# Optimization experiments

Measured on AMD Instinct MI355X. Metric: run time of the kernel, lower is better.

The kernel has to match this reference:

```python
import jax, jax.numpy as jnp
import numpy as np

CODEBOOK_SIZE = 1024
CODEBOOK_DIM = 64
COMMITMENT_WEIGHT = 0.25
DECAY = 0.99
EPS = 1e-5


def setup_inputs() -> dict:
    key = jax.random.key(0)
    k1, k2, k3 = jax.random.split(key, 3)
    B, D, T = 32, CODEBOOK_DIM, 4096
    z = jax.random.normal(k1, (B, D, T), dtype=jnp.float32)
    embedding = jax.random.normal(k2, (CODEBOOK_SIZE, CODEBOOK_DIM), dtype=jnp.float32)
    cluster_size = jnp.zeros((CODEBOOK_SIZE,), dtype=jnp.float32)
    embed_avg = jax.random.normal(k3, (CODEBOOK_SIZE, CODEBOOK_DIM), dtype=jnp.float32)
    return {"z": z, "embedding": embedding, "cluster_size": cluster_size, "embed_avg": embed_avg}


def reference(z, embedding, cluster_size, embed_avg):
    # z: [B, D, T]; embedding/embed_avg: [K, D]; cluster_size: [K]
    B, D, T = z.shape
    K = embedding.shape[0]
    z_flat = jnp.transpose(z, (0, 2, 1)).reshape(-1, D)  # [N, D], N = B*T

    # squared-euclidean distances via expansion (matches torch cdist expansion)
    dist = (
        jnp.sum(z_flat * z_flat, axis=1, keepdims=True)
        + jnp.sum(embedding * embedding, axis=1)
        - 2.0 * (z_flat @ embedding.T)
    )  # [N, K]
    indices = jnp.argmin(dist, axis=1)  # [N] int

    # EMA updates (training path). one_hot.sum(0) -> segment count; one_hot.T @ z_flat -> segment sum
    counts = jax.ops.segment_sum(jnp.ones(z_flat.shape[0], dtype=z_flat.dtype), indices, num_segments=K)
    new_cluster_size = cluster_size * DECAY + (1.0 - DECAY) * counts
    embed_sum = jax.ops.segment_sum(z_flat, indices, num_segments=K)  # [K, D]
    new_embed_avg = embed_avg * DECAY + (1.0 - DECAY) * embed_sum
    n = jnp.sum(new_cluster_size)
    smoothed = (new_cluster_size + EPS) / (n + K * EPS) * n  # Laplace smoothing
    new_embedding = new_embed_avg / smoothed[:, None]  # [K, D]

    # quantize with the *updated* codebook (as in the torch in-place update)
    z_q_flat = new_embedding[indices]  # [N, D] gather
    loss = COMMITMENT_WEIGHT * jnp.mean((z_flat - jax.lax.stop_gradient(z_q_flat)) ** 2)
    # straight-through estimator
    z_q_flat = z_flat + jax.lax.stop_gradient(z_q_flat - z_flat)
    z_q = jnp.transpose(z_q_flat.reshape(B, T, D), (0, 2, 1))  # [B, D, T]
    return z_q, loss, indices.reshape(B, T)
```

## Files before the change

kernel.cpp:

```cpp
#include <hip/hip_runtime.h>

#define N_PTS 131072
#define TD 4096
#define DD 64
#define KK 1024
#define MARGIN_TH 2e-3f

typedef short bf16x8 __attribute__((ext_vector_type(8)));
typedef float f32x4  __attribute__((ext_vector_type(4)));

__device__ inline unsigned short f2bf(float f) {
    unsigned u = __float_as_uint(f);
    unsigned r = u + 0x7FFFu + ((u >> 16) & 1u);
    return (unsigned short)(r >> 16);
}
__device__ inline float bf2f(unsigned short h) {
    return __uint_as_float(((unsigned)h) << 16);
}

__device__ inline void gload_lds16(const unsigned short* g, unsigned short* l) {
    __builtin_amdgcn_global_load_lds(
        (const __attribute__((address_space(1))) unsigned int*)g,
        (__attribute__((address_space(3))) unsigned int*)l, 16, 0, 0);
}

__global__ __launch_bounds__(256) void vq_prep(const float* __restrict__ z,
                                               unsigned short* __restrict__ zh,
                                               unsigned short* __restrict__ zl)
{
    __shared__ float tile[64][65];
    const int tid = threadIdx.x;
    const int b = blockIdx.x >> 6;
    const int t0 = (blockIdx.x & 63) * 64;

    const int d = tid >> 2, tq = tid & 3;
#pragma unroll
    for (int it = 0; it < 4; ++it) {
        const int tt = tq * 16 + it * 4;
        const float4 v = *(const float4*)(z + ((size_t)b * DD + d) * TD + t0 + tt);
        tile[d][tt] = v.x; tile[d][tt + 1] = v.y; tile[d][tt + 2] = v.z; tile[d][tt + 3] = v.w;
    }
    __syncthreads();

    const int p = tid >> 2, dg = tid & 3;
    bf16x8 h0, h1, l0, l1;
#pragma unroll
    for (int j = 0; j < 8; ++j) {
        const float v0 = -tile[dg * 16 + j][p];
        const unsigned short a = f2bf(v0);
        h0[j] = (short)a; l0[j] = (short)f2bf(v0 - bf2f(a));
        const float v1 = -tile[dg * 16 + 8 + j][p];
        const unsigned short c = f2bf(v1);
        h1[j] = (short)c; l1[j] = (short)f2bf(v1 - bf2f(c));
    }
    const size_t o = ((size_t)(b * TD + t0 + p)) * DD + dg * 16;
    *(bf16x8*)(zh + o) = h0;
    *(bf16x8*)(zh + o + 8) = h1;
    *(bf16x8*)(zl + o) = l0;
    *(bf16x8*)(zl + o + 8) = l1;
}

__global__ __launch_bounds__(256) void vq_eprep(const float* __restrict__ emb,
                                                unsigned short* __restrict__ eh,
                                                unsigned short* __restrict__ el,
                                                float* __restrict__ halfnorm)
{
    const int k = blockIdx.x * 256 + threadIdx.x;
    if (k >= KK) return;
    const float* e = emb + (size_t)k * DD;
    double s = 0.0;
#pragma unroll
    for (int d = 0; d < DD; ++d) {
        const float v = e[d];
        const double dv = (double)v;
        s = fma(dv, dv, s);
        const unsigned short h = f2bf(v);
        eh[(size_t)k * DD + d] = h;
        el[(size_t)k * DD + d] = f2bf(v - bf2f(h));
    }
    halfnorm[k] = (float)(0.5 * s);
}

__global__ __launch_bounds__(256, 4) void vq_screen_mfma(
    const unsigned short* __restrict__ zh, const unsigned short* __restrict__ zl,
    const unsigned short* __restrict__ eh, const unsigned short* __restrict__ el,
    const float* __restrict__ hn,
    int* __restrict__ idx_ws, float* __restrict__ ind_out,
    int* __restrict__ nflag, int* __restrict__ flags, int* __restrict__ hist)
{
    __shared__ __align__(16) unsigned short ehs[2][1024];
    __shared__ __align__(16) unsigned short els[2][1024];

    const int tid  = threadIdx.x;
    const int lane = tid & 63;
    const int wv   = tid >> 6;
    const int quad = lane >> 4;
    const int col  = lane & 15;
    const int pbase = blockIdx.x * 128 + wv * 32;

    const bf16x8* pA0h = (const bf16x8*)(zh + (size_t)(pbase + col) * DD + quad * 8);
    const bf16x8* pA0l = (const bf16x8*)(zl + (size_t)(pbase + col) * DD + quad * 8);
    const bf16x8* pA1h = (const bf16x8*)(zh + (size_t)(pbase + 16 + col) * DD + quad * 8);
    const bf16x8* pA1l = (const bf16x8*)(zl + (size_t)(pbase + 16 + col) * DD + quad * 8);
    const bf16x8 A0h0 = pA0h[0], A0h1 = pA0h[4];
    const bf16x8 A0l0 = pA0l[0], A0l1 = pA0l[4];
    const bf16x8 A1h0 = pA1h[0], A1h1 = pA1h[4];
    const bf16x8 A1l0 = pA1l[0], A1l1 = pA1l[4];

    const int ci = tid & 127;
    const int sc = ci >> 3, sm = ci & 7;
    const int sj = (sm - sc) & 7;
    const unsigned short* sgl = (tid < 128 ? eh : el) + sc * DD + sj * 8;
    unsigned short* dst0 = (tid < 128 ? &ehs[0][0] : &els[0][0]) + (wv & 1) * 512 + lane * 8;
    unsigned short* dst1 = dst0 + 1024;

    const int pH0 = (col * 8 + ((quad + col) & 7)) * 8;
    const int pH1 = (col * 8 + ((quad + 4 + col) & 7)) * 8;

    gload_lds16(sgl, dst0);
    float hnv_c = hn[col];
    float hnv_n = hnv_c;
    __syncthreads();

    float best0[4]  = {1e30f, 1e30f, 1e30f, 1e30f};
    float best20[4] = {1e30f, 1e30f, 1e30f, 1e30f};
    int   bidx0[4]  = {0, 0, 0, 0};
    float best1[4]  = {1e30f, 1e30f, 1e30f, 1e30f};
    float best21[4] = {1e30f, 1e30f, 1e30f, 1e30f};
    int   bidx1[4]  = {0, 0, 0, 0};

    int code = col;
#pragma unroll 2
    for (int t = 0; t < KK / 16; ++t) {
        const int cur = t & 1;
        if (t < 63) {
            gload_lds16(sgl + (t + 1) * (16 * DD), cur ? dst0 : dst1);
            hnv_n = hn[(t + 1) * 16 + col];
        }

        const unsigned short* bh = &ehs[cur][0];
        const unsigned short* bl = &els[cur][0];
        const bf16x8 Bh0 = *(const bf16x8*)(bh + pH0);
        const bf16x8 Bh1 = *(const bf16x8*)(bh + pH1);
        const bf16x8 Bl0 = *(const bf16x8*)(bl + pH0);
        const bf16x8 Bl1 = *(const bf16x8*)(bl + pH1);

        f32x4 a0 = {hnv_c, hnv_c, hnv_c, hnv_c};
        f32x4 a1 = {hnv_c, hnv_c, hnv_c, hnv_c};
        a0 = __builtin_amdgcn_mfma_f32_16x16x32_bf16(A0h0, Bh0, a0, 0, 0, 0);
        a1 = __builtin_amdgcn_mfma_f32_16x16x32_bf16(A1h0, Bh0, a1, 0, 0, 0);
        a0 = __builtin_amdgcn_mfma_f32_16x16x32_bf16(A0h1, Bh1, a0, 0, 0, 0);
        a1 = __builtin_amdgcn_mfma_f32_16x16x32_bf16(A1h1, Bh1, a1, 0, 0, 0);
        a0 = __builtin_amdgcn_mfma_f32_16x16x32_bf16(A0l0, Bh0, a0, 0, 0, 0);
        a1 = __builtin_amdgcn_mfma_f32_16x16x32_bf16(A1l0, Bh0, a1, 0, 0, 0);
        a0 = __builtin_amdgcn_mfma_f32_16x16x32_bf16(A0l1, Bh1, a0, 0, 0, 0);
        a1 = __builtin_amdgcn_mfma_f32_16x16x32_bf16(A1l1, Bh1, a1, 0, 0, 0);
        a0 = __builtin_amdgcn_mfma_f32_16x16x32_bf16(A0h0, Bl0, a0, 0, 0, 0);
        a1 = __builtin_amdgcn_mfma_f32_16x16x32_bf16(A1h0, Bl0, a1, 0, 0, 0);
        a0 = __builtin_amdgcn_mfma_f32_16x16x32_bf16(A0h1, Bl1, a0, 0, 0, 0);
        a1 = __builtin_amdgcn_mfma_f32_16x16x32_bf16(A1h1, Bl1, a1, 0, 0, 0);

#pragma unroll
        for (int r = 0; r < 4; ++r) {
            const float s0 = a0[r];
            best20[r] = __builtin_amdgcn_fmed3f(best0[r], best20[r], s0);
            if (s0 < best0[r]) { best0[r] = s0; bidx0[r] = code; }
            const float s1 = a1[r];
            best21[r] = __builtin_amdgcn_fmed3f(best1[r], best21[r], s1);
            if (s1 < best1[r]) { best1[r] = s1; bidx1[r] = code; }
        }

        __syncthreads();
        hnv_c = hnv_n;
        code += 16;
    }

#pragma unroll
    for (int off = 1; off < 16; off <<= 1) {
#pragma unroll
        for (int r = 0; r < 4; ++r) {
            {
                const float ob  = __shfl_xor(best0[r],  off, 64);
                const float ob2 = __shfl_xor(best20[r], off, 64);
                const int   oi  = __shfl_xor(bidx0[r],  off, 64);
                const float nb2 = fminf(fminf(best20[r], ob2), fmaxf(best0[r], ob));
                if (ob < best0[r]) { best0[r] = ob; bidx0[r] = oi; }
                best20[r] = nb2;
            }
            {
                const float ob  = __shfl_xor(best1[r],  off, 64);
                const float ob2 = __shfl_xor(best21[r], off, 64);
                const int   oi  = __shfl_xor(bidx1[r],  off, 64);
                const float nb2 = fminf(fminf(best21[r], ob2), fmaxf(best1[r], ob));
                if (ob < best1[r]) { best1[r] = ob; bidx1[r] = oi; }
                best21[r] = nb2;
            }
        }
    }

    if (col == 0) {
#pragma unroll
        for (int r = 0; r < 4; ++r) {
            const int n0 = pbase + quad * 4 + r;
            idx_ws[n0] = bidx0[r];
            ind_out[n0] = (float)bidx0[r];
            atomicAdd(&hist[bidx0[r]], 1);
            if (best20[r] - best0[r] < MARGIN_TH) {
                const int pos = atomicAdd(nflag, 1);
                flags[pos] = n0;
            }
            const int n1 = pbase + 16 + quad * 4 + r;
            idx_ws[n1] = bidx1[r];
            ind_out[n1] = (float)bidx1[r];
            atomicAdd(&hist[bidx1[r]], 1);
            if (best21[r] - best1[r] < MARGIN_TH) {
                const int pos = atomicAdd(nflag, 1);
                flags[pos] = n1;
            }
        }
    }
}

__global__ __launch_bounds__(256) void vq_fallback(
    const float* __restrict__ z, const float* __restrict__ emb,
    int* __restrict__ idx_ws, float* __restrict__ ind_out,
    const int* __restrict__ nflag, const int* __restrict__ flags,
    int* __restrict__ hist)
{
    __shared__ float zs[4][DD];
    const int total = *nflag;
    const int lane = threadIdx.x & 63;
    const int wid = threadIdx.x >> 6;
    const int gw = blockIdx.x * 4 + wid;

    for (int i = gw; i < total; i += gridDim.x * 4) {
        const int n = flags[i];
        const int b = n >> 12, t = n & 4095;
        zs[wid][lane] = z[((size_t)b * DD + lane) * TD + t];
        __builtin_amdgcn_s_waitcnt(0);
        double best = 1e300;
        int bi = KK;
        for (int kc = 0; kc < KK / 64; ++kc) {
            const int k = kc * 64 + lane;
            const float4* e = (const float4*)(emb + (size_t)k * DD);
            double dot = 0.0, nn = 0.0;
#pragma unroll
            for (int j = 0; j < 16; ++j) {
                float4 ev = e[j];
                double e0 = (double)ev.x, e1 = (double)ev.y, e2 = (double)ev.z, e3 = (double)ev.w;
                nn = fma(e0, e0, fma(e1, e1, fma(e2, e2, fma(e3, e3, nn))));
                dot = fma((double)zs[wid][4 * j + 0], e0,
                      fma((double)zs[wid][4 * j + 1], e1,
                      fma((double)zs[wid][4 * j + 2], e2,
                      fma((double)zs[wid][4 * j + 3], e3, dot))));
            }
            double s = 0.5 * nn - dot;
            if (s < best || (s == best && k < bi)) { best = s; bi = k; }
        }
        for (int off = 32; off > 0; off >>= 1) {
            double os = __shfl_down(best, off, 64);
            int oi = __shfl_down(bi, off, 64);
            if (os < best || (os == best && oi < bi)) { best = os; bi = oi; }
        }
        if (lane == 0) {
            const int old = idx_ws[n];
            if (bi != old) {
                idx_ws[n] = bi;
                ind_out[n] = (float)bi;
                atomicAdd(&hist[old], -1);
                atomicAdd(&hist[bi], 1);
            }
        }
    }
}

__global__ __launch_bounds__(1024) void vq_prefix_smo(
    const int* __restrict__ hist, const float* __restrict__ cs,
    int* __restrict__ cursor, float* __restrict__ rsmo)
{
    __shared__ int tmp[KK];
    __shared__ double dred[KK];
    const int k = threadIdx.x;
    const int c = hist[k];
    tmp[k] = c;
    const double ncs = 0.99 * (double)cs[k] + 0.01 * (double)c;
    dred[k] = ncs;
    __syncthreads();
    for (int off = 1; off < KK; off <<= 1) {
        int u = (k >= off) ? tmp[k - off] : 0;
        __syncthreads();
        tmp[k] += u;
        __syncthreads();
    }
    cursor[k] = tmp[k] - c;
    for (int s = 512; s > 0; s >>= 1) {
        if (k < s) dred[k] += dred[k + s];
        __syncthreads();
    }
    const double nsum = dred[0];
    const double smo = (ncs + 1e-5) / (nsum + (double)KK * 1e-5) * nsum;
    rsmo[k] = (float)(1.0 / smo);
}

__global__ __launch_bounds__(256) void vq_scatter(const int* __restrict__ idx_ws,
                                                  int* __restrict__ cursor, int* __restrict__ order)
{
    const int n = blockIdx.x * 256 + threadIdx.x;
    const int bi = idx_ws[n];
    const int pos = atomicAdd(&cursor[bi], 1);
    order[pos] = n;
}

__global__ __launch_bounds__(256) void vq_esum2(
    const unsigned short* __restrict__ zh, const unsigned short* __restrict__ zl,
    const int* __restrict__ idx_ws, const int* __restrict__ order,
    float* __restrict__ esum)
{
    const int tid = threadIdx.x;
    const int lane = tid & 63;
    const int w = tid >> 6;
    const int base = blockIdx.x * 256 + w * 64;

    const int pid_l = order[base + lane];
    const int code_l = idx_ws[pid_l];

    float v[64];
#pragma unroll
    for (int j = 0; j < 64; ++j) {
        const int pj = __shfl(pid_l, j, 64);
        const size_t o = (size_t)pj * DD + lane;
        v[j] = bf2f(zh[o]) + bf2f(zl[o]);
    }

    float racc = 0.f;
    int cur = __shfl(code_l, 0, 64);
#pragma unroll
    for (int j = 0; j < 64; ++j) {
        const int cj = __shfl(code_l, j, 64);
        if (cj != cur) {
            atomicAdd(&esum[(size_t)cur * DD + lane], -racc);
            racc = 0.f;
            cur = cj;
        }
        racc += v[j];
    }
    atomicAdd(&esum[(size_t)cur * DD + lane], -racc);
}

__global__ __launch_bounds__(256) void vq_newE(
    const float* __restrict__ avg, const float* __restrict__ esum,
    const float* __restrict__ rsmo, float* __restrict__ newE)
{
    const int j = blockIdx.x * 256 + threadIdx.x;
    newE[j] = (float)((0.99 * (double)avg[j] + 0.01 * (double)esum[j]) * (double)rsmo[j >> 6]);
}

__global__ __launch_bounds__(256) void vq_gather_loss(
    const float* __restrict__ z, const float* __restrict__ newE,
    const int* __restrict__ idx_ws, float* __restrict__ zq_out,
    double* __restrict__ loss_acc, int* __restrict__ done_cnt,
    float* __restrict__ loss_out)
{
    const int tid = threadIdx.x;
    const int n = blockIdx.x * 256 + tid;
    const int b = n >> 12;
    const int t = n & 4095;
    const float* zb = z + ((size_t)b * DD) * TD + t;
    float* ob = zq_out + ((size_t)b * DD) * TD + t;
    const int bi = idx_ws[n];
    const float* e = newE + (size_t)bi * DD;
    double acc = 0.0;
#pragma unroll
    for (int d = 0; d < DD; ++d) {
        float q = e[d];
        float zv = zb[(size_t)d * TD];
        ob[(size_t)d * TD] = q;
        float df = zv - q;
        acc = fma((double)df, (double)df, acc);
    }
    for (int off = 32; off > 0; off >>= 1) acc += __shfl_down(acc, off, 64);
    __shared__ double wsum[4];
    const int wid = tid >> 6, lane = tid & 63;
    if (lane == 0) wsum[wid] = acc;
    __syncthreads();
    if (tid == 0) {
        atomicAdd(loss_acc, wsum[0] + wsum[1] + wsum[2] + wsum[3]);
        __threadfence();
        const int prev = atomicAdd(done_cnt, 1);
        if (prev == gridDim.x - 1) {
            __threadfence();
            *loss_out = (float)(0.25 * (*loss_acc) / (double)(N_PTS * DD));
        }
    }
}

extern "C" void kernel_launch(void* const* d_in, const int* in_sizes, int n_in,
                              void* d_out, int out_size, void* d_ws, size_t ws_size,
                              hipStream_t stream) {
    const float* z    = (const float*)d_in[0];
    const float* emb  = (const float*)d_in[1];
    const float* cs   = (const float*)d_in[2];
    const float* avg  = (const float*)d_in[3];

    float* out      = (float*)d_out;
    float* zq_out   = out;
    float* loss_out = out + 8388608;
    float* ind_out  = out + 8388609;

    unsigned short* zh = (unsigned short*)d_out;
    unsigned short* zl = (unsigned short*)((char*)d_out + 16777216);

    char* ws = (char*)d_ws;
    int*            idx_ws   = (int*)ws;
    float*          newE     = (float*)(ws + 524288);
    float*          esum     = (float*)(ws + 786432);
    int*            hist     = (int*)(ws + 1048576);
    int*            nflag    = (int*)(ws + 1052672);
    int*            done_cnt = (int*)(ws + 1052676);
    double*         loss_acc = (double*)(ws + 1052680);
    float*          halfnorm = (float*)(ws + 1052688);
    int*            cursor   = (int*)(ws + 1056784);
    int*            flags    = (int*)(ws + 1060880);
    int*            order    = (int*)(ws + 1585168);
    unsigned short* eh       = (unsigned short*)(ws + 2109456);
    unsigned short* el       = (unsigned short*)(ws + 2240528);
    float*          rsmo     = (float*)(ws + 2371600);

    hipMemsetAsync(ws + 786432, 0, 266256, stream);

    vq_prep<<<2048, 256, 0, stream>>>(z, zh, zl);
    vq_eprep<<<4, 256, 0, stream>>>(emb, eh, el, halfnorm);
    vq_screen_mfma<<<1024, 256, 0, stream>>>(zh, zl, eh, el, halfnorm,
                                             idx_ws, ind_out, nflag, flags, hist);
    vq_fallback<<<128, 256, 0, stream>>>(z, emb, idx_ws, ind_out, nflag, flags, hist);
    vq_prefix_smo<<<1, 1024, 0, stream>>>(hist, cs, cursor, rsmo);
    vq_scatter<<<N_PTS / 256, 256, 0, stream>>>(idx_ws, cursor, order);
    vq_esum2<<<N_PTS / 256, 256, 0, stream>>>(zh, zl, idx_ws, order, esum);
    vq_newE<<<256, 256, 0, stream>>>(avg, esum, rsmo, newE);
    vq_gather_loss<<<N_PTS / 256, 256, 0, stream>>>(z, newE, idx_ws, zq_out,
                                                    loss_acc, done_cnt, loss_out);
}
```

Baseline: 332.8 us.

## Pre-swizzle codebook into MFMA fragment layout and load directly to registers

The codebook prep kernel now writes the bf16 hi/lo embedding split in a layout that matches the MFMA B-operand fragment per 16-code tile. The screening kernel drops the LDS double buffer, its global_load_lds staging and the per-iteration __syncthreads. Each lane instead prefetches its next tile's fragments from global memory (L2-resident) into registers one iteration ahead. This removes the block-wide barriers and LDS traffic, but every wave now fetches the codebook separately from cache, which adds global/L2 load pressure and latency exposure.

```diff
diff --git a/kernel.cpp b/kernel.cpp
--- a/kernel.cpp
+++ b/kernel.cpp
@@ -16,12 +16,6 @@
 }
 __device__ inline float bf2f(unsigned short h) {
     return __uint_as_float(((unsigned)h) << 16);
-}
-
-__device__ inline void gload_lds16(const unsigned short* g, unsigned short* l) {
-    __builtin_amdgcn_global_load_lds(
-        (const __attribute__((address_space(1))) unsigned int*)g,
-        (__attribute__((address_space(3))) unsigned int*)l, 16, 0, 0);
 }
 
 __global__ __launch_bounds__(256) void vq_prep(const float* __restrict__ z,
@@ -61,12 +55,13 @@
 }
 
 __global__ __launch_bounds__(256) void vq_eprep(const float* __restrict__ emb,
-                                                unsigned short* __restrict__ eh,
-                                                unsigned short* __restrict__ el,
+                                                unsigned short* __restrict__ efh,
+                                                unsigned short* __restrict__ efl,
                                                 float* __restrict__ halfnorm)
 {
     const int k = blockIdx.x * 256 + threadIdx.x;
     if (k >= KK) return;
+    const int t = k >> 4, col = k & 15;
     const float* e = emb + (size_t)k * DD;
     double s = 0.0;
 #pragma unroll
@@ -75,22 +70,21 @@
         const double dv = (double)v;
         s = fma(dv, dv, s);
         const unsigned short h = f2bf(v);
-        eh[(size_t)k * DD + d] = h;
-        el[(size_t)k * DD + d] = f2bf(v - bf2f(h));
+        const int q = d >> 3, j = d & 7;
+        const size_t pos = (size_t)t * 1024 + (q >> 2) * 512 + ((q & 3) * 16 + col) * 8 + j;
+        efh[pos] = h;
+        efl[pos] = f2bf(v - bf2f(h));
     }
     halfnorm[k] = (float)(0.5 * s);
 }
 
 __global__ __launch_bounds__(256, 4) void vq_screen_mfma(
     const unsigned short* __restrict__ zh, const unsigned short* __restrict__ zl,
-    const unsigned short* __restrict__ eh, const unsigned short* __restrict__ el,
+    const unsigned short* __restrict__ efh, const unsigned short* __restrict__ efl,
     const float* __restrict__ hn,
     int* __restrict__ idx_ws, float* __restrict__ ind_out,
     int* __restrict__ nflag, int* __restrict__ flags, int* __restrict__ hist)
 {
-    __shared__ __align__(16) unsigned short ehs[2][1024];
-    __shared__ __align__(16) unsigned short els[2][1024];
-
     const int tid  = threadIdx.x;
     const int lane = tid & 63;
     const int wv   = tid >> 6;
@@ -107,20 +101,14 @@
     const bf16x8 A1h0 = pA1h[0], A1h1 = pA1h[4];
     const bf16x8 A1l0 = pA1l[0], A1l1 = pA1l[4];
 
-    const int ci = tid & 127;
-    const int sc = ci >> 3, sm = ci & 7;
-    const int sj = (sm - sc) & 7;
-    const unsigned short* sgl = (tid < 128 ? eh : el) + sc * DD + sj * 8;
-    unsigned short* dst0 = (tid < 128 ? &ehs[0][0] : &els[0][0]) + (wv & 1) * 512 + lane * 8;
-    unsigned short* dst1 = dst0 + 1024;
-
-    const int pH0 = (col * 8 + ((quad + col) & 7)) * 8;
-    const int pH1 = (col * 8 + ((quad + 4 + col) & 7)) * 8;
-
-    gload_lds16(sgl, dst0);
-    float hnv_c = hn[col];
-    float hnv_n = hnv_c;
-    __syncthreads();
+    const unsigned short* fh = efh + lane * 8;
+    const unsigned short* fl = efl + lane * 8;
+
+    bf16x8 ch0 = *(const bf16x8*)(fh);
+    bf16x8 ch1 = *(const bf16x8*)(fh + 512);
+    bf16x8 cl0 = *(const bf16x8*)(fl);
+    bf16x8 cl1 = *(const bf16x8*)(fl + 512);
+    float chn = hn[col];
 
     float best0[4]  = {1e30f, 1e30f, 1e30f, 1e30f};
     float best20[4] = {1e30f, 1e30f, 1e30f, 1e30f};
@@ -129,37 +117,31 @@
     float best21[4] = {1e30f, 1e30f, 1e30f, 1e30f};
     int   bidx1[4]  = {0, 0, 0, 0};
 
-    int code = col;
 #pragma unroll 2
     for (int t = 0; t < KK / 16; ++t) {
-        const int cur = t & 1;
-        if (t < 63) {
-            gload_lds16(sgl + (t + 1) * (16 * DD), cur ? dst0 : dst1);
-            hnv_n = hn[(t + 1) * 16 + col];
-        }
-
-        const unsigned short* bh = &ehs[cur][0];
-        const unsigned short* bl = &els[cur][0];
-        const bf16x8 Bh0 = *(const bf16x8*)(bh + pH0);
-        const bf16x8 Bh1 = *(const bf16x8*)(bh + pH1);
-        const bf16x8 Bl0 = *(const bf16x8*)(bl + pH0);
-        const bf16x8 Bl1 = *(const bf16x8*)(bl + pH1);
-
-        f32x4 a0 = {hnv_c, hnv_c, hnv_c, hnv_c};
-        f32x4 a1 = {hnv_c, hnv_c, hnv_c, hnv_c};
-        a0 = __builtin_amdgcn_mfma_f32_16x16x32_bf16(A0h0, Bh0, a0, 0, 0, 0);
-        a1 = __builtin_amdgcn_mfma_f32_16x16x32_bf16(A1h0, Bh0, a1, 0, 0, 0);
-        a0 = __builtin_amdgcn_mfma_f32_16x16x32_bf16(A0h1, Bh1, a0, 0, 0, 0);
-        a1 = __builtin_amdgcn_mfma_f32_16x16x32_bf16(A1h1, Bh1, a1, 0, 0, 0);
-        a0 = __builtin_amdgcn_mfma_f32_16x16x32_bf16(A0l0, Bh0, a0, 0, 0, 0);
-        a1 = __builtin_amdgcn_mfma_f32_16x16x32_bf16(A1l0, Bh0, a1, 0, 0, 0);
-        a0 = __builtin_amdgcn_mfma_f32_16x16x32_bf16(A0l1, Bh1, a0, 0, 0, 0);
-        a1 = __builtin_amdgcn_mfma_f32_16x16x32_bf16(A1l1, Bh1, a1, 0, 0, 0);
-        a0 = __builtin_amdgcn_mfma_f32_16x16x32_bf16(A0h0, Bl0, a0, 0, 0, 0);
-        a1 = __builtin_amdgcn_mfma_f32_16x16x32_bf16(A1h0, Bl0, a1, 0, 0, 0);
-        a0 = __builtin_amdgcn_mfma_f32_16x16x32_bf16(A0h1, Bl1, a0, 0, 0, 0);
-        a1 = __builtin_amdgcn_mfma_f32_16x16x32_bf16(A1h1, Bl1, a1, 0, 0, 0);
-
+        const int tn = (t + 1) & 63;
+        const bf16x8 nh0 = *(const bf16x8*)(fh + tn * 1024);
+        const bf16x8 nh1 = *(const bf16x8*)(fh + tn * 1024 + 512);
+        const bf16x8 nl0 = *(const bf16x8*)(fl + tn * 1024);
+        const bf16x8 nl1 = *(const bf16x8*)(fl + tn * 1024 + 512);
+        const float  nhn = hn[tn * 16 + col];
+
+        f32x4 a0 = {chn, chn, chn, chn};
+        f32x4 a1 = {chn, chn, chn, chn};
+        a0 = __builtin_amdgcn_mfma_f32_16x16x32_bf16(A0h0, ch0, a0, 0, 0, 0);
+        a1 = __builtin_amdgcn_mfma_f32_16x16x32_bf16(A1h0, ch0, a1, 0, 0, 0);
+        a0 = __builtin_amdgcn_mfma_f32_16x16x32_bf16(A0h1, ch1, a0, 0, 0, 0);
+        a1 = __builtin_amdgcn_mfma_f32_16x16x32_bf16(A1h1, ch1, a1, 0, 0, 0);
+        a0 = __builtin_amdgcn_mfma_f32_16x16x32_bf16(A0l0, ch0, a0, 0, 0, 0);
+        a1 = __builtin_amdgcn_mfma_f32_16x16x32_bf16(A1l0, ch0, a1, 0, 0, 0);
+        a0 = __builtin_amdgcn_mfma_f32_16x16x32_bf16(A0l1, ch1, a0, 0, 0, 0);
+        a1 = __builtin_amdgcn_mfma_f32_16x16x32_bf16(A1l1, ch1, a1, 0, 0, 0);
+        a0 = __builtin_amdgcn_mfma_f32_16x16x32_bf16(A0h0, cl0, a0, 0, 0, 0);
+        a1 = __builtin_amdgcn_mfma_f32_16x16x32_bf16(A1h0, cl0, a1, 0, 0, 0);
+        a0 = __builtin_amdgcn_mfma_f32_16x16x32_bf16(A0h1, cl1, a0, 0, 0, 0);
+        a1 = __builtin_amdgcn_mfma_f32_16x16x32_bf16(A1h1, cl1, a1, 0, 0, 0);
+
+        const int code = t * 16 + col;
 #pragma unroll
         for (int r = 0; r < 4; ++r) {
             const float s0 = a0[r];
@@ -170,9 +152,7 @@
             if (s1 < best1[r]) { best1[r] = s1; bidx1[r] = code; }
         }
 
-        __syncthreads();
-        hnv_c = hnv_n;
-        code += 16;
+        ch0 = nh0; ch1 = nh1; cl0 = nl0; cl1 = nl1; chn = nhn;
     }
 
 #pragma unroll
@@ -422,15 +402,15 @@
     int*            cursor   = (int*)(ws + 1056784);
     int*            flags    = (int*)(ws + 1060880);
     int*            order    = (int*)(ws + 1585168);
-    unsigned short* eh       = (unsigned short*)(ws + 2109456);
-    unsigned short* el       = (unsigned short*)(ws + 2240528);
+    unsigned short* efh      = (unsigned short*)(ws + 2109456);
+    unsigned short* efl      = (unsigned short*)(ws + 2240528);
     float*          rsmo     = (float*)(ws + 2371600);
 
     hipMemsetAsync(ws + 786432, 0, 266256, stream);
 
     vq_prep<<<2048, 256, 0, stream>>>(z, zh, zl);
-    vq_eprep<<<4, 256, 0, stream>>>(emb, eh, el, halfnorm);
-    vq_screen_mfma<<<1024, 256, 0, stream>>>(zh, zl, eh, el, halfnorm,
+    vq_eprep<<<4, 256, 0, stream>>>(emb, efh, efl, halfnorm);
+    vq_screen_mfma<<<1024, 256, 0, stream>>>(zh, zl, efh, efl, halfnorm,
                                              idx_ws, ind_out, nflag, flags, hist);
     vq_fallback<<<128, 256, 0, stream>>>(z, emb, idx_ws, ind_out, nflag, flags, hist);
     vq_prefix_smo<<<1, 1024, 0, stream>>>(hist, cs, cursor, rsmo);
```

Result: slower. 342.0 us (+2.8%).
